# Performance work log

Measured on AMD Instinct MI355X. Metric: run time of the kernel, lower is better.

Reference implementation:

```python
import jax, jax.numpy as jnp
import numpy as np

N_NODES = 200000
F = 256
B = 8192
FAN1 = 16  # hop-1 fanout (layer_num_samples[0])
FAN2 = 4   # hop-2 fanout (layer_num_samples[1])


def setup_inputs() -> dict:
    key = jax.random.key(0)
    k1, k2, k3, k4, k5, k6 = jax.random.split(key, 6)
    node_feats = jax.random.normal(k1, (N_NODES, F), dtype=jnp.float32)
    # SageLayer weight: [out_size, 2*layer_size]
    W1 = jax.random.normal(k2, (F, 2 * F), dtype=jnp.float32) * 0.05
    W2 = jax.random.normal(k3, (F, 2 * F), dtype=jnp.float32) * 0.05
    batch_nodes = jax.random.randint(k4, (B,), 0, N_NODES)
    neigh1 = jax.random.randint(k5, (B, FAN1), 0, N_NODES)
    M1 = B + B * FAN1  # layer-1 node set: batch nodes + their sampled neighbors
    neigh2 = jax.random.randint(k6, (M1, FAN2), 0, N_NODES)
    return {"node_feats": node_feats, "W1": W1, "W2": W2,
            "batch_nodes": batch_nodes, "neigh1": neigh1, "neigh2": neigh2}


def reference(node_feats, W1, W2, batch_nodes, neigh1, neigh2):
    b = batch_nodes.shape[0]
    # layer-1 node list: batch nodes first, then hop-1 neighbors (row-major)
    nodes1 = jnp.concatenate([batch_nodes, neigh1.reshape(-1)])  # [17B]
    # ---- SAGE layer 1: MEAN-aggregate hop-2 neighbor raw features ----
    agg1 = node_feats[neigh2].mean(axis=1)              # [17B, F]
    self1 = node_feats[nodes1]                           # [17B, F]
    h1 = jax.nn.relu(jnp.concatenate([self1, agg1], axis=1) @ W1.T)  # [17B, F]
    # ---- SAGE layer 2: MEAN-aggregate hop-1 neighbors' hidden embs ----
    agg2 = h1[b:].reshape(b, neigh1.shape[1], -1).mean(axis=1)  # [B, F]
    h_self = h1[:b]                                      # [B, F]
    out = jax.nn.relu(jnp.concatenate([h_self, agg2], axis=1) @ W2.T)  # [B, F]
    return out
```

## Files before the change

### kernel.cpp

```cpp
#include <hip/hip_runtime.h>
#include <hip/hip_bf16.h>

#define NB 8192
#define M1T 139264
#define SELFB 128
#define NFEAT 51200000

typedef __attribute__((ext_vector_type(8))) short bf16x8;
typedef __attribute__((ext_vector_type(16))) float f32x16;
typedef __attribute__((ext_vector_type(4))) float f32x4;

__device__ __forceinline__ unsigned short f2b(float f) {
  union { float f; unsigned u; } v; v.f = f;
  unsigned r = v.u + 0x7fffu + ((v.u >> 16) & 1u);
  return (unsigned short)(r >> 16);
}
__device__ __forceinline__ float b2f(unsigned u16) {
  union { unsigned u; float f; } v; v.u = u16 << 16;
  return v.f;
}
__device__ __forceinline__ uint4 pack8u(float a0, float a1, float a2, float a3,
                                        float a4, float a5, float a6, float a7) {
  uint4 v;
  v.x = (unsigned)f2b(a0) | ((unsigned)f2b(a1) << 16);
  v.y = (unsigned)f2b(a2) | ((unsigned)f2b(a3) << 16);
  v.z = (unsigned)f2b(a4) | ((unsigned)f2b(a5) << 16);
  v.w = (unsigned)f2b(a6) | ((unsigned)f2b(a7) << 16);
  return v;
}

#define GLDS16(g, l)                                                          \
  __builtin_amdgcn_global_load_lds(                                           \
      (const __attribute__((address_space(1))) unsigned int*)(const void*)(g),\
      (__attribute__((address_space(3))) unsigned int*)(void*)(l), 16, 0, 0)

__global__ void convert_w(const float* __restrict__ W1, const float* __restrict__ W2,
                          unsigned short* __restrict__ W1s, unsigned short* __restrict__ W2s) {
  int i = blockIdx.x * 256 + threadIdx.x;
  const float* W; unsigned short* out; int f4;
  if (i < 32768) { W = W1; out = W1s; f4 = i; }
  else           { W = W2; out = W2s; f4 = i - 32768; }
  int n  = (f4 * 4) >> 9;
  int c0 = (f4 * 4) & 511;
  int kt = c0 >> 6;
  int slot = (c0 & 63) >> 3;
  int e  = c0 & 7;
  int sw = slot ^ (n & 7);
  f32x4 v = *((const f32x4*)W + f4);
  ushort4 o;
  o.x = f2b(v[0]); o.y = f2b(v[1]); o.z = f2b(v[2]); o.w = f2b(v[3]);
  *(ushort4*)(out + kt * 16384 + n * 64 + sw * 8 + e) = o;
}

__global__ __launch_bounds__(256)
void conv_feats(const float* __restrict__ feats, unsigned short* __restrict__ featsb) {
  const int stride = gridDim.x * 256;
  for (size_t s = (size_t)blockIdx.x * 256 + threadIdx.x; s < NFEAT / 8; s += stride) {
    const f32x4* p = (const f32x4*)feats + s * 2;
    f32x4 x = __builtin_nontemporal_load(p);
    f32x4 y = __builtin_nontemporal_load(p + 1);
    *((uint4*)featsb + s) = pack8u(x[0], x[1], x[2], x[3], y[0], y[1], y[2], y[3]);
  }
}

__global__ __launch_bounds__(512, 4)
void sage_l1_bf(const unsigned short* __restrict__ featsb,
                const unsigned short* __restrict__ Wbs,
                const int* __restrict__ batch_nodes,
                const int* __restrict__ neigh1,
                const int* __restrict__ neigh2,
                unsigned short* __restrict__ A2)
{
  __shared__ __align__(16) unsigned short As[2][64 * 64];
  __shared__ __align__(16) unsigned short Bs[2][256 * 64];
  const int tid = threadIdx.x;
  const int m0 = blockIdx.x * 64;
  const int w = tid >> 6, lane = tid & 63, l31 = lane & 31, lh = lane >> 5;
  const int mh = w & 1, nq = w >> 1;
  const int m = tid >> 3, slot = tid & 7;
  const int r = m0 + m;

  const int self = (r < NB) ? batch_nodes[r] : neigh1[r - NB];
  const int4 nb = *(const int4*)(neigh2 + (size_t)r * 4);
  const char* fb = (const char*)featsb;
  const unsigned so  = (unsigned)self * 512u + (unsigned)slot * 16u;
  const unsigned no0 = (unsigned)nb.x * 512u + (unsigned)slot * 16u;
  const unsigned no1 = (unsigned)nb.y * 512u + (unsigned)slot * 16u;
  const unsigned no2 = (unsigned)nb.z * 512u + (unsigned)slot * 16u;
  const unsigned no3 = (unsigned)nb.w * 512u + (unsigned)slot * 16u;
  const int arowC = mh * 32 + l31;
  const int n0C = nq * 64 + l31, n1C = n0C + 32;

  f32x16 acc0 = {}, acc1 = {};
  uint4 a0[4], a1[4];

  #define L1_LOADS(KT, AR)                                                    \
    do { if ((KT) < 4) {                                                      \
           AR[0] = *(const uint4*)(fb + so + (KT) * 128);                     \
         } else {                                                             \
           const int _kb = ((KT) - 4) * 128;                                  \
           AR[0] = *(const uint4*)(fb + no0 + _kb);                           \
           AR[1] = *(const uint4*)(fb + no1 + _kb);                           \
           AR[2] = *(const uint4*)(fb + no2 + _kb);                           \
           AR[3] = *(const uint4*)(fb + no3 + _kb);                           \
         } } while (0)

  #define L1_BISSUE(KT)                                                       \
    do { const unsigned short* _s = Wbs + (size_t)(KT) * 16384;               \
         unsigned short* _d = &Bs[(KT) & 1][0];                               \
         _Pragma("unroll")                                                    \
         for (int _q = 0; _q < 4; ++_q) {                                     \
           int _i = _q * 512 + tid;                                           \
           GLDS16(_s + (size_t)_i * 8, _d + _i * 8);                          \
         } } while (0)

  #define L1_CONV(KT, AR, AV)                                                 \
    do { if ((KT) < 4) { AV = AR[0]; }                                        \
         else {                                                               \
           float s0 = 0, s1 = 0, s2 = 0, s3 = 0, s4 = 0, s5 = 0, s6 = 0, s7 = 0; \
           _Pragma("unroll")                                                  \
           for (int _j = 0; _j < 4; ++_j) {                                   \
             s0 += b2f(AR[_j].x & 0xffffu); s1 += b2f(AR[_j].x >> 16);        \
             s2 += b2f(AR[_j].y & 0xffffu); s3 += b2f(AR[_j].y >> 16);        \
             s4 += b2f(AR[_j].z & 0xffffu); s5 += b2f(AR[_j].z >> 16);        \
             s6 += b2f(AR[_j].w & 0xffffu); s7 += b2f(AR[_j].w >> 16);        \
           }                                                                  \
           AV = pack8u(s0 * 0.25f, s1 * 0.25f, s2 * 0.25f, s3 * 0.25f,        \
                       s4 * 0.25f, s5 * 0.25f, s6 * 0.25f, s7 * 0.25f);       \
         } } while (0)

  #define L1_STEP(KT, AR, NCNT)                                               \
    do { uint4 _av;                                                           \
         L1_CONV(KT, AR, _av);      \
         *(uint4*)(&As[(KT) & 1][m * 64 + ((slot ^ (m & 7)) << 3)]) = _av;    \
         asm volatile("s_waitcnt vmcnt(" #NCNT ") lgkmcnt(0)" ::: "memory");  \
         __builtin_amdgcn_s_barrier();                                        \
         if ((KT) < 7) L1_BISSUE((KT) + 1);                                   \
         if ((KT) < 6) L1_LOADS((KT) + 2, AR);                                \
         __builtin_amdgcn_sched_barrier(0);                                   \
         __builtin_amdgcn_s_setprio(1);                                       \
         _Pragma("unroll")                                                    \
         for (int _kk = 0; _kk < 4; ++_kk) {                                  \
           int _sl = _kk * 2 + lh;                                            \
           bf16x8 _a  = *(const bf16x8*)(&As[(KT) & 1][arowC * 64 + ((_sl ^ (arowC & 7)) << 3)]); \
           bf16x8 _b0 = *(const bf16x8*)(&Bs[(KT) & 1][n0C * 64 + ((_sl ^ (n0C & 7)) << 3)]);     \
           bf16x8 _b1 = *(const bf16x8*)(&Bs[(KT) & 1][n1C * 64 + ((_sl ^ (n1C & 7)) << 3)]);     \
           acc0 = __builtin_amdgcn_mfma_f32_32x32x16_bf16(_a, _b0, acc0, 0, 0, 0);                \
           acc1 = __builtin_amdgcn_mfma_f32_32x32x16_bf16(_a, _b1, acc1, 0, 0, 0);                \
         }                                                                    \
         __builtin_amdgcn_s_setprio(0);                                       \
    } while (0)

  L1_LOADS(0, a0);
  L1_BISSUE(0);
  L1_LOADS(1, a1);
  __builtin_amdgcn_sched_barrier(0);

  L1_STEP(0, a0, 1);
  L1_STEP(1, a1, 1);
  L1_STEP(2, a0, 1);
  L1_STEP(3, a1, 4);
  L1_STEP(4, a0, 4);
  L1_STEP(5, a1, 4);
  L1_STEP(6, a0, 4);
  L1_STEP(7, a1, 0);

  #undef L1_LOADS
  #undef L1_BISSUE
  #undef L1_CONV
  #undef L1_STEP

  if (blockIdx.x < SELFB) {
    #pragma unroll
    for (int q = 0; q < 16; ++q) {
      int row = m0 + mh * 32 + (q & 3) + 8 * (q >> 2) + 4 * lh;
      int col0 = nq * 64 + l31;
      float v0 = acc0[q], v1 = acc1[q];
      v0 = v0 > 0.f ? v0 : 0.f;
      v1 = v1 > 0.f ? v1 : 0.f;
      A2[(size_t)row * 512 + col0] = f2b(v0);
      A2[(size_t)row * 512 + col0 + 32] = f2b(v1);
    }
  } else {
    const int bi = blockIdx.x - SELFB;
    #pragma unroll
    for (int gi = 0; gi < 2; ++gi) {
      float sA = 0.f, sB = 0.f;
      #pragma unroll
      for (int q = gi * 8; q < gi * 8 + 8; ++q) {
        float v0 = acc0[q], v1 = acc1[q];
        sA += (v0 > 0.f ? v0 : 0.f);
        sB += (v1 > 0.f ? v1 : 0.f);
      }
      sA += __shfl_xor(sA, 32, 64);
      sB += __shfl_xor(sB, 32, 64);
      if (lh == 0) {
        int gr = bi * 4 + mh * 2 + gi;
        int col = 256 + nq * 64 + l31;
        A2[(size_t)gr * 512 + col] = f2b(sA * 0.0625f);
        A2[(size_t)gr * 512 + col + 32] = f2b(sB * 0.0625f);
      }
    }
  }
}

__global__ __launch_bounds__(512, 4)
void sage_l1_f32(const float* __restrict__ feats,
                 const unsigned short* __restrict__ Wbs,
                 const int* __restrict__ batch_nodes,
                 const int* __restrict__ neigh1,
                 const int* __restrict__ neigh2,
                 unsigned short* __restrict__ A2)
{
  __shared__ __align__(16) unsigned short As[2][64 * 64];
  __shared__ __align__(16) unsigned short Bs[2][256 * 64];
  const int tid = threadIdx.x;
  const int m0 = blockIdx.x * 64;
  const int w = tid >> 6, lane = tid & 63, l31 = lane & 31, lh = lane >> 5;
  const int mh = w & 1, nq = w >> 1;
  const int m = tid >> 3, slot = tid & 7;
  const int r = m0 + m;

  const int self = (r < NB) ? batch_nodes[r] : neigh1[r - NB];
  const int4 nb = *(const int4*)(neigh2 + (size_t)r * 4);
  const char* fb = (const char*)feats;
  const unsigned so  = (unsigned)self * 1024u + (unsigned)slot * 32u;
  const unsigned no0 = (unsigned)nb.x * 1024u + (unsigned)slot * 32u;
  const unsigned no1 = (unsigned)nb.y * 1024u + (unsigned)slot * 32u;
  const unsigned no2 = (unsigned)nb.z * 1024u + (unsigned)slot * 32u;
  const unsigned no3 = (unsigned)nb.w * 1024u + (unsigned)slot * 32u;
  const int arowC = mh * 32 + l31;
  const int n0C = nq * 64 + l31, n1C = n0C + 32;

  f32x16 acc0 = {}, acc1 = {};
  f32x4 a0[8], a1[8];

  #define L1F_LOADS(KT, AR)                                                   \
    do { if ((KT) < 4) {                                                      \
           AR[0] = *(const f32x4*)(fb + so + (KT) * 256);                     \
           AR[1] = *(const f32x4*)(fb + so + (KT) * 256 + 16);                \
         } else {                                                             \
           const int _kb = ((KT) - 4) * 256;                                  \
           AR[0] = *(const f32x4*)(fb + no0 + _kb);                           \
           AR[1] = *(const f32x4*)(fb + no0 + _kb + 16);                      \
           AR[2] = *(const f32x4*)(fb + no1 + _kb);                           \
           AR[3] = *(const f32x4*)(fb + no1 + _kb + 16);                      \
           AR[4] = *(const f32x4*)(fb + no2 + _kb);                           \
           AR[5] = *(const f32x4*)(fb + no2 + _kb + 16);                      \
           AR[6] = *(const f32x4*)(fb + no3 + _kb);                           \
           AR[7] = *(const f32x4*)(fb + no3 + _kb + 16);                      \
         } } while (0)

  #define L1F_BISSUE(KT)                                                      \
    do { const unsigned short* _s = Wbs + (size_t)(KT) * 16384;               \
         unsigned short* _d = &Bs[(KT) & 1][0];                               \
         _Pragma("unroll")                                                    \
         for (int _q = 0; _q < 4; ++_q) {                                     \
           int _i = _q * 512 + tid;                                           \
           GLDS16(_s + (size_t)_i * 8, _d + _i * 8);                          \
         } } while (0)

  #define L1F_CONV(KT, AR, AV)                                                \
    do { if ((KT) < 4) {                                                      \
           AV = pack8u(AR[0][0], AR[0][1], AR[0][2], AR[0][3],                \
                       AR[1][0], AR[1][1], AR[1][2], AR[1][3]);               \
         } else {                                                             \
           float s0 = AR[0][0] + AR[2][0] + AR[4][0] + AR[6][0];              \
           float s1 = AR[0][1] + AR[2][1] + AR[4][1] + AR[6][1];              \
           float s2 = AR[0][2] + AR[2][2] + AR[4][2] + AR[6][2];              \
           float s3 = AR[0][3] + AR[2][3] + AR[4][3] + AR[6][3];              \
           float s4 = AR[1][0] + AR[3][0] + AR[5][0] + AR[7][0];              \
           float s5 = AR[1][1] + AR[3][1] + AR[5][1] + AR[7][1];              \
           float s6 = AR[1][2] + AR[3][2] + AR[5][2] + AR[7][2];              \
           float s7 = AR[1][3] + AR[3][3] + AR[5][3] + AR[7][3];              \
           AV = pack8u(s0 * 0.25f, s1 * 0.25f, s2 * 0.25f, s3 * 0.25f,        \
                       s4 * 0.25f, s5 * 0.25f, s6 * 0.25f, s7 * 0.25f);       \
         } } while (0)

  #define L1F_STEP(KT, AR, NCNT)                                              \
    do { uint4 _av;                                                           \
         L1F_CONV(KT, AR, _av);                                               \
         *(uint4*)(&As[(KT) & 1][m * 64 + ((slot ^ (m & 7)) << 3)]) = _av;    \
         asm volatile("s_waitcnt vmcnt(" #NCNT ") lgkmcnt(0)" ::: "memory");  \
         __builtin_amdgcn_s_barrier();                                        \
         if ((KT) < 7) L1F_BISSUE((KT) + 1);                                  \
         if ((KT) < 6) L1F_LOADS((KT) + 2, AR);                               \
         __builtin_amdgcn_sched_barrier(0);                                   \
         __builtin_amdgcn_s_setprio(1);                                       \
         _Pragma("unroll")                                                    \
         for (int _kk = 0; _kk < 4; ++_kk) {                                  \
           int _sl = _kk * 2 + lh;                                            \
           bf16x8 _a  = *(const bf16x8*)(&As[(KT) & 1][arowC * 64 + ((_sl ^ (arowC & 7)) << 3)]); \
           bf16x8 _b0 = *(const bf16x8*)(&Bs[(KT) & 1][n0C * 64 + ((_sl ^ (n0C & 7)) << 3)]);     \
           bf16x8 _b1 = *(const bf16x8*)(&Bs[(KT) & 1][n1C * 64 + ((_sl ^ (n1C & 7)) << 3)]);     \
           acc0 = __builtin_amdgcn_mfma_f32_32x32x16_bf16(_a, _b0, acc0, 0, 0, 0);                \
           acc1 = __builtin_amdgcn_mfma_f32_32x32x16_bf16(_a, _b1, acc1, 0, 0, 0);                \
         }                                                                    \
         __builtin_amdgcn_s_setprio(0);                                       \
    } while (0)

  L1F_LOADS(0, a0);
  L1F_BISSUE(0);
  L1F_LOADS(1, a1);
  __builtin_amdgcn_sched_barrier(0);

  L1F_STEP(0, a0, 2);
  L1F_STEP(1, a1, 2);
  L1F_STEP(2, a0, 2);
  L1F_STEP(3, a1, 8);
  L1F_STEP(4, a0, 8);
  L1F_STEP(5, a1, 8);
  L1F_STEP(6, a0, 8);
  L1F_STEP(7, a1, 0);

  #undef L1F_LOADS
  #undef L1F_BISSUE
  #undef L1F_CONV
  #undef L1F_STEP

  if (blockIdx.x < SELFB) {
    #pragma unroll
    for (int q = 0; q < 16; ++q) {
      int row = m0 + mh * 32 + (q & 3) + 8 * (q >> 2) + 4 * lh;
      int col0 = nq * 64 + l31;
      float v0 = acc0[q], v1 = acc1[q];
      v0 = v0 > 0.f ? v0 : 0.f;
      v1 = v1 > 0.f ? v1 : 0.f;
      A2[(size_t)row * 512 + col0] = f2b(v0);
      A2[(size_t)row * 512 + col0 + 32] = f2b(v1);
    }
  } else {
    const int bi = blockIdx.x - SELFB;
    #pragma unroll
    for (int gi = 0; gi < 2; ++gi) {
      float sA = 0.f, sB = 0.f;
      #pragma unroll
      for (int q = gi * 8; q < gi * 8 + 8; ++q) {
        float v0 = acc0[q], v1 = acc1[q];
        sA += (v0 > 0.f ? v0 : 0.f);
        sB += (v1 > 0.f ? v1 : 0.f);
      }
      sA += __shfl_xor(sA, 32, 64);
      sB += __shfl_xor(sB, 32, 64);
      if (lh == 0) {
        int gr = bi * 4 + mh * 2 + gi;
        int col = 256 + nq * 64 + l31;
        A2[(size_t)gr * 512 + col] = f2b(sA * 0.0625f);
        A2[(size_t)gr * 512 + col + 32] = f2b(sB * 0.0625f);
      }
    }
  }
}

__global__ __launch_bounds__(256, 2)
void sage_l2(const unsigned short* __restrict__ A2,
             const unsigned short* __restrict__ Wbs,
             float* __restrict__ out)
{
  __shared__ __align__(16) unsigned short As[2][32 * 64];
  __shared__ __align__(16) unsigned short Bs[2][256 * 64];
  const int tid = threadIdx.x;
  const int m0 = blockIdx.x * 32;
  const int w = tid >> 6, lane = tid & 63, l31 = lane & 31, lh = lane >> 5;
  const int mA = tid >> 3, swA = tid & 7;
  const int arowC = l31;
  const int n0C = w * 64 + l31, n1C = n0C + 32;
  const unsigned short* aSrc = A2 + (size_t)(m0 + mA) * 512 + (swA ^ (mA & 7)) * 8;

  f32x16 acc0 = {}, acc1 = {};

  #define L2_STAGE(KT)                                                        \
    do { const unsigned short* _s = Wbs + (size_t)(KT) * 16384;               \
         unsigned short* _d = &Bs[(KT) & 1][0];                               \
         _Pragma("unroll")                                                    \
         for (int _q = 0; _q < 8; ++_q) {                                     \
           int _i = _q * 256 + tid;                                           \
           GLDS16(_s + (size_t)_i * 8, _d + _i * 8);                          \
         }                                                                    \
         GLDS16(aSrc + (KT) * 64, &As[(KT) & 1][mA * 64 + swA * 8]);          \
    } while (0)

  L2_STAGE(0);
  asm volatile("s_waitcnt vmcnt(0)" ::: "memory");
  __builtin_amdgcn_s_barrier();

  #pragma unroll
  for (int kt = 0; kt < 8; ++kt) {
    if (kt < 7) L2_STAGE(kt + 1);
    __builtin_amdgcn_s_setprio(1);
    #pragma unroll
    for (int kk = 0; kk < 4; ++kk) {
      int sl = kk * 2 + lh;
      bf16x8 a  = *(const bf16x8*)(&As[kt & 1][arowC * 64 + ((sl ^ (arowC & 7)) << 3)]);
      bf16x8 b0 = *(const bf16x8*)(&Bs[kt & 1][n0C * 64 + ((sl ^ (n0C & 7)) << 3)]);
      bf16x8 b1 = *(const bf16x8*)(&Bs[kt & 1][n1C * 64 + ((sl ^ (n1C & 7)) << 3)]);
      acc0 = __builtin_amdgcn_mfma_f32_32x32x16_bf16(a, b0, acc0, 0, 0, 0);
      acc1 = __builtin_amdgcn_mfma_f32_32x32x16_bf16(a, b1, acc1, 0, 0, 0);
    }
    __builtin_amdgcn_s_setprio(0);
    asm volatile("s_waitcnt vmcnt(0)" ::: "memory");
    __builtin_amdgcn_s_barrier();
  }
  #undef L2_STAGE

  #pragma unroll
  for (int q = 0; q < 16; ++q) {
    int row = m0 + (q & 3) + 8 * (q >> 2) + 4 * lh;
    float v0 = acc0[q], v1 = acc1[q];
    out[(size_t)row * 256 + n0C] = v0 > 0.f ? v0 : 0.f;
    out[(size_t)row * 256 + n1C] = v1 > 0.f ? v1 : 0.f;
  }
}

extern "C" void kernel_launch(void* const* d_in, const int* in_sizes, int n_in,
                              void* d_out, int out_size, void* d_ws, size_t ws_size,
                              hipStream_t stream) {
  const float* feats       = (const float*)d_in[0];
  const float* W1          = (const float*)d_in[1];
  const float* W2          = (const float*)d_in[2];
  const int*   batch_nodes = (const int*)d_in[3];
  const int*   neigh1      = (const int*)d_in[4];
  const int*   neigh2      = (const int*)d_in[5];
  float* out = (float*)d_out;

  unsigned short* W1s   = (unsigned short*)d_ws;
  unsigned short* W2s   = W1s + 131072;
  unsigned short* A2    = W2s + 131072;
  unsigned short* featsb = A2 + (size_t)NB * 512;

  const size_t need = ((size_t)131072 * 2 + (size_t)NB * 512 + (size_t)NFEAT) * 2;

  hipLaunchKernelGGL(convert_w, dim3(256), dim3(256), 0, stream, W1, W2, W1s, W2s);
  if (ws_size >= need) {
    hipLaunchKernelGGL(conv_feats, dim3(3200), dim3(256), 0, stream, feats, featsb);
    hipLaunchKernelGGL(sage_l1_bf, dim3(M1T / 64), dim3(512), 0, stream,
                       featsb, W1s, batch_nodes, neigh1, neigh2, A2);
  } else {
    hipLaunchKernelGGL(sage_l1_f32, dim3(M1T / 64), dim3(512), 0, stream,
                       feats, W1s, batch_nodes, neigh1, neigh2, A2);
  }
  hipLaunchKernelGGL(sage_l2, dim3(NB / 32), dim3(256), 0, stream, A2, W2s, out);
}
```

Before: 141.6 us.

## Halve layer-1 weight K-tile to 32 and raise occupancy to 6 blocks

Splits the layer-1 GEMM's weight staging into 32-wide K tiles with a new swizzled bf16 layout, so the B shared buffer shrinks from 64 KB to 32 KB. Launch bounds go from 4 to 6 blocks per CU. The pipeline now runs 16 half-steps, and the A gather/convert happens only on even steps. The intent is higher occupancy to better hide the random gather latency, at the cost of twice as many barriers and a larger weight-conversion workspace.

```diff
diff --git a/kernel.cpp b/kernel.cpp
--- a/kernel.cpp
+++ b/kernel.cpp
@@ -35,21 +35,28 @@
       (__attribute__((address_space(3))) unsigned int*)(void*)(l), 16, 0, 0)
 
 __global__ void convert_w(const float* __restrict__ W1, const float* __restrict__ W2,
-                          unsigned short* __restrict__ W1s, unsigned short* __restrict__ W2s) {
+                          unsigned short* __restrict__ W1s32,
+                          unsigned short* __restrict__ W1s64,
+                          unsigned short* __restrict__ W2s64) {
   int i = blockIdx.x * 256 + threadIdx.x;
-  const float* W; unsigned short* out; int f4;
-  if (i < 32768) { W = W1; out = W1s; f4 = i; }
-  else           { W = W2; out = W2s; f4 = i - 32768; }
+  const float* W; int f4;
+  if (i < 32768) { W = W1; f4 = i; }
+  else           { W = W2; f4 = i - 32768; }
   int n  = (f4 * 4) >> 9;
   int c0 = (f4 * 4) & 511;
-  int kt = c0 >> 6;
-  int slot = (c0 & 63) >> 3;
-  int e  = c0 & 7;
-  int sw = slot ^ (n & 7);
   f32x4 v = *((const f32x4*)W + f4);
   ushort4 o;
   o.x = f2b(v[0]); o.y = f2b(v[1]); o.z = f2b(v[2]); o.w = f2b(v[3]);
-  *(ushort4*)(out + kt * 16384 + n * 64 + sw * 8 + e) = o;
+  int kt64 = c0 >> 6, s8 = (c0 & 63) >> 3, e = c0 & 7;
+  int off64 = kt64 * 16384 + n * 64 + ((s8 ^ (n & 7)) << 3) + e;
+  if (i < 32768) {
+    *(ushort4*)(W1s64 + off64) = o;
+    int kt32 = c0 >> 5, s4 = (c0 >> 3) & 3;
+    int off32 = kt32 * 8192 + n * 32 + (((s4 ^ ((n >> 1) & 3))) << 3) + e;
+    *(ushort4*)(W1s32 + off32) = o;
+  } else {
+    *(ushort4*)(W2s64 + off64) = o;
+  }
 }
 
 __global__ __launch_bounds__(256)
@@ -63,16 +70,16 @@
   }
 }
 
-__global__ __launch_bounds__(512, 4)
-void sage_l1_bf(const unsigned short* __restrict__ featsb,
-                const unsigned short* __restrict__ Wbs,
-                const int* __restrict__ batch_nodes,
-                const int* __restrict__ neigh1,
-                const int* __restrict__ neigh2,
-                unsigned short* __restrict__ A2)
+__global__ __launch_bounds__(512, 6)
+void sage_l1_bf32(const unsigned short* __restrict__ featsb,
+                  const unsigned short* __restrict__ Wbs,
+                  const int* __restrict__ batch_nodes,
+                  const int* __restrict__ neigh1,
+                  const int* __restrict__ neigh2,
+                  unsigned short* __restrict__ A2)
 {
   __shared__ __align__(16) unsigned short As[2][64 * 64];
-  __shared__ __align__(16) unsigned short Bs[2][256 * 64];
+  __shared__ __align__(16) unsigned short Bs[2][256 * 32];
   const int tid = threadIdx.x;
   const int m0 = blockIdx.x * 64;
   const int w = tid >> 6, lane = tid & 63, l31 = lane & 31, lh = lane >> 5;
@@ -90,65 +97,79 @@
   const unsigned no3 = (unsigned)nb.w * 512u + (unsigned)slot * 16u;
   const int arowC = mh * 32 + l31;
   const int n0C = nq * 64 + l31, n1C = n0C + 32;
+  const int bsw0 = (n0C >> 1) & 3, bsw1 = (n1C >> 1) & 3;
 
   f32x16 acc0 = {}, acc1 = {};
   uint4 a0[4], a1[4];
 
-  #define L1_LOADS(KT, AR)                                                    \
-    do { if ((KT) < 4) {                                                      \
-           AR[0] = *(const uint4*)(fb + so + (KT) * 128);                     \
+  #define L1_LOADS(P, AR)                                                     \
+    do { if ((P) < 4) {                                                       \
+           AR[0] = *(const uint4*)(fb + so + (P) * 128);                      \
          } else {                                                             \
-           const int _kb = ((KT) - 4) * 128;                                  \
+           const int _kb = ((P) - 4) * 128;                                   \
            AR[0] = *(const uint4*)(fb + no0 + _kb);                           \
            AR[1] = *(const uint4*)(fb + no1 + _kb);                           \
            AR[2] = *(const uint4*)(fb + no2 + _kb);                           \
            AR[3] = *(const uint4*)(fb + no3 + _kb);                           \
          } } while (0)
 
-  #define L1_BISSUE(KT)                                                       \
-    do { const unsigned short* _s = Wbs + (size_t)(KT) * 16384;               \
-         unsigned short* _d = &Bs[(KT) & 1][0];                               \
-         _Pragma("unroll")                                                    \
-         for (int _q = 0; _q < 4; ++_q) {                                     \
-           int _i = _q * 512 + tid;                                           \
-           GLDS16(_s + (size_t)_i * 8, _d + _i * 8);                          \
-         } } while (0)
-
-  #define L1_CONV(KT, AR, AV)                                                 \
-    do { if ((KT) < 4) { AV = AR[0]; }                                        \
-         else {                                                               \
+  #define L1_BISSUE(KT)                                                      \
+    do { const unsigned short* _s = Wbs + (size_t)(KT) * 8192;               \
+         unsigned short* _d = &Bs[(KT) & 1][0];                              \
+         GLDS16(_s + (size_t)tid * 8, _d + tid * 8);                         \
+         GLDS16(_s + (size_t)(512 + tid) * 8, _d + (512 + tid) * 8);         \
+    } while (0)
+
+  #define L1_CONV(P, AR, AV)                                                 \
+    do { if ((P) < 4) { AV = AR[0]; }                                        \
+         else {                                                              \
            float s0 = 0, s1 = 0, s2 = 0, s3 = 0, s4 = 0, s5 = 0, s6 = 0, s7 = 0; \
-           _Pragma("unroll")                                                  \
-           for (int _j = 0; _j < 4; ++_j) {                                   \
-             s0 += b2f(AR[_j].x & 0xffffu); s1 += b2f(AR[_j].x >> 16);        \
-             s2 += b2f(AR[_j].y & 0xffffu); s3 += b2f(AR[_j].y >> 16);        \
-             s4 += b2f(AR[_j].z & 0xffffu); s5 += b2f(AR[_j].z >> 16);        \
-             s6 += b2f(AR[_j].w & 0xffffu); s7 += b2f(AR[_j].w >> 16);        \
-           }                                                                  \
-           AV = pack8u(s0 * 0.25f, s1 * 0.25f, s2 * 0.25f, s3 * 0.25f,        \
-                       s4 * 0.25f, s5 * 0.25f, s6 * 0.25f, s7 * 0.25f);       \
-         } } while (0)
-
-  #define L1_STEP(KT, AR, NCNT)                                               \
-    do { uint4 _av;                                                           \
-         L1_CONV(KT, AR, _av);      \
-         *(uint4*)(&As[(KT) & 1][m * 64 + ((slot ^ (m & 7)) << 3)]) = _av;    \
-         asm volatile("s_waitcnt vmcnt(" #NCNT ") lgkmcnt(0)" ::: "memory");  \
-         __builtin_amdgcn_s_barrier();                                        \
-         if ((KT) < 7) L1_BISSUE((KT) + 1);                                   \
-         if ((KT) < 6) L1_LOADS((KT) + 2, AR);                                \
-         __builtin_amdgcn_sched_barrier(0);                                   \
-         __builtin_amdgcn_s_setprio(1);                                       \
-         _Pragma("unroll")                                                    \
-         for (int _kk = 0; _kk < 4; ++_kk) {                                  \
-           int _sl = _kk * 2 + lh;                                            \
-           bf16x8 _a  = *(const bf16x8*)(&As[(KT) & 1][arowC * 64 + ((_sl ^ (arowC & 7)) << 3)]); \
-           bf16x8 _b0 = *(const bf16x8*)(&Bs[(KT) & 1][n0C * 64 + ((_sl ^ (n0C & 7)) << 3)]);     \
-           bf16x8 _b1 = *(const bf16x8*)(&Bs[(KT) & 1][n1C * 64 + ((_sl ^ (n1C & 7)) << 3)]);     \
-           acc0 = __builtin_amdgcn_mfma_f32_32x32x16_bf16(_a, _b0, acc0, 0, 0, 0);                \
-           acc1 = __builtin_amdgcn_mfma_f32_32x32x16_bf16(_a, _b1, acc1, 0, 0, 0);                \
-         }                                                                    \
-         __builtin_amdgcn_s_setprio(0);                                       \
+           _Pragma("unroll")                                                 \
+           for (int _j = 0; _j < 4; ++_j) {                                  \
+             s0 += b2f(AR[_j].x & 0xffffu); s1 += b2f(AR[_j].x >> 16);       \
+             s2 += b2f(AR[_j].y & 0xffffu); s3 += b2f(AR[_j].y >> 16);       \
+             s4 += b2f(AR[_j].z & 0xffffu); s5 += b2f(AR[_j].z >> 16);       \
+             s6 += b2f(AR[_j].w & 0xffffu); s7 += b2f(AR[_j].w >> 16);       \
+           }                                                                 \
+           AV = pack8u(s0 * 0.25f, s1 * 0.25f, s2 * 0.25f, s3 * 0.25f,       \
+                       s4 * 0.25f, s5 * 0.25f, s6 * 0.25f, s7 * 0.25f);      \
+         } } while (0)
+
+  #define L1_MFMA(KT)                                                        \
+    do { const int _pa = ((KT) >> 1) & 1;                                    \
+         _Pragma("unroll")                                                   \
+         for (int _kk = 0; _kk < 2; ++_kk) {                                 \
+           int _sA = ((KT) & 1) * 4 + _kk * 2 + lh;                          \
+           int _sB = _kk * 2 + lh;                                           \
+           bf16x8 _a  = *(const bf16x8*)(&As[_pa][arowC * 64 + ((_sA ^ (arowC & 7)) << 3)]); \
+           bf16x8 _b0 = *(const bf16x8*)(&Bs[(KT) & 1][n0C * 32 + ((_sB ^ bsw0) << 3)]);     \
+           bf16x8 _b1 = *(const bf16x8*)(&Bs[(KT) & 1][n1C * 32 + ((_sB ^ bsw1) << 3)]);     \
+           acc0 = __builtin_amdgcn_mfma_f32_32x32x16_bf16(_a, _b0, acc0, 0, 0, 0);           \
+           acc1 = __builtin_amdgcn_mfma_f32_32x32x16_bf16(_a, _b1, acc1, 0, 0, 0);           \
+         } } while (0)
+
+  #define STEP_E(KT, P, AR, NCNT, DOLOAD)                                    \
+    do { uint4 _av;                                                          \
+         L1_CONV(P, AR, _av);                                                \
+         *(uint4*)(&As[(P) & 1][m * 64 + ((slot ^ (m & 7)) << 3)]) = _av;    \
+         asm volatile("s_waitcnt vmcnt(" #NCNT ") lgkmcnt(0)" ::: "memory"); \
+         __builtin_amdgcn_s_barrier();                                       \
+         L1_BISSUE((KT) + 1);                                                \
+         if (DOLOAD) L1_LOADS((P) + 2, AR);                                  \
+         __builtin_amdgcn_sched_barrier(0);                                  \
+         __builtin_amdgcn_s_setprio(1);                                      \
+         L1_MFMA(KT);                                                        \
+         __builtin_amdgcn_s_setprio(0);                                      \
+    } while (0)
+
+  #define STEP_O(KT, NCNT, DOB)                                              \
+    do { asm volatile("s_waitcnt vmcnt(" #NCNT ") lgkmcnt(0)" ::: "memory"); \
+         __builtin_amdgcn_s_barrier();                                       \
+         if (DOB) L1_BISSUE((KT) + 1);                                       \
+         __builtin_amdgcn_sched_barrier(0);                                  \
+         __builtin_amdgcn_s_setprio(1);                                      \
+         L1_MFMA(KT);                                                        \
+         __builtin_amdgcn_s_setprio(0);                                      \
     } while (0)
 
   L1_LOADS(0, a0);
@@ -156,19 +177,29 @@
   L1_LOADS(1, a1);
   __builtin_amdgcn_sched_barrier(0);
 
-  L1_STEP(0, a0, 1);
-  L1_STEP(1, a1, 1);
-  L1_STEP(2, a0, 1);
-  L1_STEP(3, a1, 4);
-  L1_STEP(4, a0, 4);
-  L1_STEP(5, a1, 4);
-  L1_STEP(6, a0, 4);
-  L1_STEP(7, a1, 0);
+  STEP_E(0, 0, a0, 1, 1);
+  STEP_O(1, 1, 1);
+  STEP_E(2, 1, a1, 0, 1);
+  STEP_O(3, 1, 1);
+  STEP_E(4, 2, a0, 0, 1);
+  STEP_O(5, 4, 1);
+  STEP_E(6, 3, a1, 0, 1);
+  STEP_O(7, 4, 1);
+  STEP_E(8, 4, a0, 0, 1);
+  STEP_O(9, 4, 1);
+  STEP_E(10, 5, a1, 0, 1);
+  STEP_O(11, 4, 1);
+  STEP_E(12, 6, a0, 0, 0);
+  STEP_O(13, 0, 1);
+  STEP_E(14, 7, a1, 0, 0);
+  STEP_O(15, 0, 0);
 
   #undef L1_LOADS
   #undef L1_BISSUE
   #undef L1_CONV
-  #undef L1_STEP
+  #undef L1_MFMA
+  #undef STEP_E
+  #undef STEP_O
 
   if (blockIdx.x < SELFB) {
     #pragma unroll
@@ -423,21 +454,23 @@
   const int*   neigh2      = (const int*)d_in[5];
   float* out = (float*)d_out;
 
-  unsigned short* W1s   = (unsigned short*)d_ws;
-  unsigned short* W2s   = W1s + 131072;
-  unsigned short* A2    = W2s + 131072;
+  unsigned short* W1s32  = (unsigned short*)d_ws;
+  unsigned short* W1s64  = W1s32 + 131072;
+  unsigned short* W2s64  = W1s64 + 131072;
+  unsigned short* A2     = W2s64 + 131072;
   unsigned short* featsb = A2 + (size_t)NB * 512;
 
-  const size_t need = ((size_t)131072 * 2 + (size_t)NB * 512 + (size_t)NFEAT) * 2;
-
-  hipLaunchKernelGGL(convert_w, dim3(256), dim3(256), 0, stream, W1, W2, W1s, W2s);
+  const size_t need = ((size_t)131072 * 3 + (size_t)NB * 512 + (size_t)NFEAT) * 2;
+
+  hipLaunchKernelGGL(convert_w, dim3(256), dim3(256), 0, stream, W1, W2,
+                     W1s32, W1s64, W2s64);
   if (ws_size >= need) {
     hipLaunchKernelGGL(conv_feats, dim3(3200), dim3(256), 0, stream, feats, featsb);
-    hipLaunchKernelGGL(sage_l1_bf, dim3(M1T / 64), dim3(512), 0, stream,
-                       featsb, W1s, batch_nodes, neigh1, neigh2, A2);
+    hipLaunchKernelGGL(sage_l1_bf32, dim3(M1T / 64), dim3(512), 0, stream,
+                       featsb, W1s32, batch_nodes, neigh1, neigh2, A2);
   } else {
     hipLaunchKernelGGL(sage_l1_f32, dim3(M1T / 64), dim3(512), 0, stream,
-                       feats, W1s, batch_nodes, neigh1, neigh2, A2);
-  }
-  hipLaunchKernelGGL(sage_l2, dim3(NB / 32), dim3(256), 0, stream, A2, W2s, out);
-}
+                       feats, W1s64, batch_nodes, neigh1, neigh2, A2);
+  }
+  hipLaunchKernelGGL(sage_l2, dim3(NB / 32), dim3(256), 0, stream, A2, W2s64, out);
+}
```

Measured after the change: 265.9 us. 87.8% more time.
